# Optimization experiments

Measured on AMD Instinct MI355X. Metric: run time of the kernel, lower is better.

## Reference

```python
import jax, jax.numpy as jnp
import numpy as np

N_FEAT = 1024
N_LAYER = 4  # n_layer + 1 in the original module


def setup_inputs() -> dict:
    key = jax.random.key(0)
    kx, kw, kb = jax.random.split(key, 3)
    x = jax.random.normal(kx, (16384, N_FEAT), dtype=jnp.float32)
    weight_w = jax.random.normal(kw, (N_LAYER, N_FEAT), dtype=jnp.float32)
    weight_b = jax.random.normal(kb, (N_LAYER, N_FEAT), dtype=jnp.float32)
    return {"x": x, "weight_w": weight_w, "weight_b": weight_b}


def reference(x, weight_w, weight_b):
    # Original per layer: x_{i+1} = x0 @ x_i^T @ w_i + b_i + x_i  (per sample).
    # (x0 x_i^T) w = x0 * <x_i, w>, so we use the O(n) equivalent form and
    # never materialize the [B, n, n] outer product.
    x0 = x  # [B, n]
    xi = x0
    for i in range(N_LAYER):
        xiw = jnp.einsum("bn,n->b", xi, weight_w[i])  # [B]
        xi = x0 * xiw[:, None] + weight_b[i][None, :] + xi
    return xi
```

## Files before the change

### kernel.cpp

```cpp
#include <hip/hip_runtime.h>

#define N_FEAT 1024
#define N_LAYER 4
#define R 8

__global__ __launch_bounds__(256) void crossnet_kernel(
    const float* __restrict__ x,
    const float* __restrict__ weight_w,
    const float* __restrict__ weight_b,
    float* __restrict__ out,
    int n_rows) {
  const int wave = threadIdx.x >> 6;
  const int lane = threadIdx.x & 63;
  const int row0 = (blockIdx.x * 4 + wave) * R;
  if (row0 >= n_rows) return;

  const float4* xq = (const float4*)x;
  float4* oq = (float4*)out;

  float4 x0[R * 4];
#pragma unroll
  for (int r = 0; r < R; ++r)
#pragma unroll
    for (int c = 0; c < 4; ++c)
      x0[r * 4 + c] = xq[(size_t)(row0 + r) * 256 + c * 64 + lane];

  float p[R * N_LAYER];
#pragma unroll
  for (int k = 0; k < R * N_LAYER; ++k) p[k] = 0.f;
  float e[N_LAYER] = {0.f, 0.f, 0.f, 0.f};
  float4 csum[4];

#pragma unroll
  for (int c = 0; c < 4; ++c) {
    float4 w[N_LAYER];
#pragma unroll
    for (int i = 0; i < N_LAYER; ++i)
      w[i] = ((const float4*)(weight_w + i * N_FEAT))[c * 64 + lane];

    float4 cum = make_float4(0.f, 0.f, 0.f, 0.f);
#pragma unroll
    for (int i = 0; i < N_LAYER; ++i) {
      if (i > 0)
        e[i] += cum.x * w[i].x + cum.y * w[i].y + cum.z * w[i].z + cum.w * w[i].w;
      float4 b = ((const float4*)(weight_b + i * N_FEAT))[c * 64 + lane];
      cum.x += b.x; cum.y += b.y; cum.z += b.z; cum.w += b.w;
    }
    csum[c] = cum;

#pragma unroll
    for (int r = 0; r < R; ++r) {
      const float4 xv = x0[r * 4 + c];
#pragma unroll
      for (int i = 0; i < N_LAYER; ++i) {
        p[r * N_LAYER + i] += xv.x * w[i].x + xv.y * w[i].y +
                              xv.z * w[i].z + xv.w * w[i].w;
      }
    }
  }

#pragma unroll
  for (int off = 32; off > 0; off >>= 1) {
#pragma unroll
    for (int k = 0; k < R * N_LAYER; ++k) p[k] += __shfl_xor(p[k], off, 64);
#pragma unroll
    for (int i = 1; i < N_LAYER; ++i) e[i] += __shfl_xor(e[i], off, 64);
  }

#pragma unroll
  for (int r = 0; r < R; ++r) {
    float A = 1.f;
#pragma unroll
    for (int i = 0; i < N_LAYER; ++i)
      A += A * p[r * N_LAYER + i] + e[i];

#pragma unroll
    for (int c = 0; c < 4; ++c) {
      const float4 xv = x0[r * 4 + c];
      float4 o;
      o.x = fmaf(xv.x, A, csum[c].x);
      o.y = fmaf(xv.y, A, csum[c].y);
      o.z = fmaf(xv.z, A, csum[c].z);
      o.w = fmaf(xv.w, A, csum[c].w);
      oq[(size_t)(row0 + r) * 256 + c * 64 + lane] = o;
    }
  }
}

extern "C" void kernel_launch(void* const* d_in, const int* in_sizes, int n_in,
                              void* d_out, int out_size, void* d_ws, size_t ws_size,
                              hipStream_t stream) {
  const float* x = (const float*)d_in[0];
  const float* ww = (const float*)d_in[1];
  const float* wb = (const float*)d_in[2];
  float* out = (float*)d_out;

  int n_rows = in_sizes[0] / N_FEAT;
  int rows_per_block = 4 * R;
  int n_blocks = (n_rows + rows_per_block - 1) / rows_per_block;
  crossnet_kernel<<<n_blocks, 256, 0, stream>>>(x, ww, wb, out, n_rows);
}
```

Measured before the change: 119.1 us.

## Split crossnet into reduction kernel and streaming elementwise output kernel

Replaces the single fused kernel, which kept each wave's rows in registers and wrote output directly, with two kernels. The first computes per-row scale factors and the bias cumsum into workspace. The second is a grid-stride elementwise pass that re-reads x and writes the output. This frees registers and gives a simple streaming second pass, at the cost of reading x from memory twice and paying an extra launch.

New measurement: 132.5 us. +11.3%, slower.

```diff
diff --git a/kernel.cpp b/kernel.cpp
--- a/kernel.cpp
+++ b/kernel.cpp
@@ -2,34 +2,39 @@
 
 #define N_FEAT 1024
 #define N_LAYER 4
-#define R 8
+#define R1 8
 
-__global__ __launch_bounds__(256) void crossnet_kernel(
+
+__global__ __launch_bounds__(256) void crossnet_phase1(
     const float* __restrict__ x,
     const float* __restrict__ weight_w,
     const float* __restrict__ weight_b,
-    float* __restrict__ out,
+    float* __restrict__ A_out,
+    float* __restrict__ csum_out,
     int n_rows) {
   const int wave = threadIdx.x >> 6;
   const int lane = threadIdx.x & 63;
-  const int row0 = (blockIdx.x * 4 + wave) * R;
+  const int row0 = (blockIdx.x * 4 + wave) * R1;
+
+  if (blockIdx.x == 0) {
+    const int t = threadIdx.x;
+    float4 c = make_float4(0.f, 0.f, 0.f, 0.f);
+#pragma unroll
+    for (int i = 0; i < N_LAYER; ++i) {
+      const float4 b = ((const float4*)(weight_b + i * N_FEAT))[t];
+      c.x += b.x; c.y += b.y; c.z += b.z; c.w += b.w;
+    }
+    ((float4*)csum_out)[t] = c;
+  }
+
   if (row0 >= n_rows) return;
 
   const float4* xq = (const float4*)x;
-  float4* oq = (float4*)out;
 
-  float4 x0[R * 4];
+  float p[R1 * N_LAYER];
 #pragma unroll
-  for (int r = 0; r < R; ++r)
-#pragma unroll
-    for (int c = 0; c < 4; ++c)
-      x0[r * 4 + c] = xq[(size_t)(row0 + r) * 256 + c * 64 + lane];
-
-  float p[R * N_LAYER];
-#pragma unroll
-  for (int k = 0; k < R * N_LAYER; ++k) p[k] = 0.f;
+  for (int k = 0; k < R1 * N_LAYER; ++k) p[k] = 0.f;
   float e[N_LAYER] = {0.f, 0.f, 0.f, 0.f};
-  float4 csum[4];
 
 #pragma unroll
   for (int c = 0; c < 4; ++c) {
@@ -43,14 +48,13 @@
     for (int i = 0; i < N_LAYER; ++i) {
       if (i > 0)
         e[i] += cum.x * w[i].x + cum.y * w[i].y + cum.z * w[i].z + cum.w * w[i].w;
-      float4 b = ((const float4*)(weight_b + i * N_FEAT))[c * 64 + lane];
+      const float4 b = ((const float4*)(weight_b + i * N_FEAT))[c * 64 + lane];
       cum.x += b.x; cum.y += b.y; cum.z += b.z; cum.w += b.w;
     }
-    csum[c] = cum;
 
 #pragma unroll
-    for (int r = 0; r < R; ++r) {
-      const float4 xv = x0[r * 4 + c];
+    for (int r = 0; r < R1; ++r) {
+      const float4 xv = xq[(size_t)(row0 + r) * 256 + c * 64 + lane];
 #pragma unroll
       for (int i = 0; i < N_LAYER; ++i) {
         p[r * N_LAYER + i] += xv.x * w[i].x + xv.y * w[i].y +
@@ -62,28 +66,44 @@
 #pragma unroll
   for (int off = 32; off > 0; off >>= 1) {
 #pragma unroll
-    for (int k = 0; k < R * N_LAYER; ++k) p[k] += __shfl_xor(p[k], off, 64);
+    for (int k = 0; k < R1 * N_LAYER; ++k) p[k] += __shfl_xor(p[k], off, 64);
 #pragma unroll
     for (int i = 1; i < N_LAYER; ++i) e[i] += __shfl_xor(e[i], off, 64);
   }
 
+  if (lane == 0) {
 #pragma unroll
-  for (int r = 0; r < R; ++r) {
-    float A = 1.f;
+    for (int r = 0; r < R1; ++r) {
+      float A = 1.f;
 #pragma unroll
-    for (int i = 0; i < N_LAYER; ++i)
-      A += A * p[r * N_LAYER + i] + e[i];
+      for (int i = 0; i < N_LAYER; ++i)
+        A += A * p[r * N_LAYER + i] + e[i];
+      A_out[row0 + r] = A;
+    }
+  }
+}
 
-#pragma unroll
-    for (int c = 0; c < 4; ++c) {
-      const float4 xv = x0[r * 4 + c];
-      float4 o;
-      o.x = fmaf(xv.x, A, csum[c].x);
-      o.y = fmaf(xv.y, A, csum[c].y);
-      o.z = fmaf(xv.z, A, csum[c].z);
-      o.w = fmaf(xv.w, A, csum[c].w);
-      oq[(size_t)(row0 + r) * 256 + c * 64 + lane] = o;
-    }
+__global__ __launch_bounds__(256) void crossnet_phase2(
+    const float* __restrict__ x,
+    const float* __restrict__ A_in,
+    const float* __restrict__ csum_in,
+    float* __restrict__ out,
+    int n_q) {
+  const float4* xq = (const float4*)x;
+  const float4* cq = (const float4*)csum_in;
+  float4* oq = (float4*)out;
+
+  const int stride = gridDim.x * 256;
+  for (int q = blockIdx.x * 256 + threadIdx.x; q < n_q; q += stride) {
+    const float a = A_in[q >> 8];
+    const float4 xv = xq[q];
+    const float4 c = cq[q & 255];
+    float4 o;
+    o.x = fmaf(xv.x, a, c.x);
+    o.y = fmaf(xv.y, a, c.y);
+    o.z = fmaf(xv.z, a, c.z);
+    o.w = fmaf(xv.w, a, c.w);
+    oq[q] = o;
   }
 }
 
@@ -95,8 +115,14 @@
   const float* wb = (const float*)d_in[2];
   float* out = (float*)d_out;
 
-  int n_rows = in_sizes[0] / N_FEAT;
-  int rows_per_block = 4 * R;
-  int n_blocks = (n_rows + rows_per_block - 1) / rows_per_block;
-  crossnet_kernel<<<n_blocks, 256, 0, stream>>>(x, ww, wb, out, n_rows);
+  const int n_rows = in_sizes[0] / N_FEAT;
+  float* A_ws = (float*)d_ws;
+  float* csum_ws = A_ws + n_rows;
+
+  const int rows_per_block = 4 * R1;
+  const int n_blocks1 = (n_rows + rows_per_block - 1) / rows_per_block;
+  crossnet_phase1<<<n_blocks1, 256, 0, stream>>>(x, ww, wb, A_ws, csum_ws, n_rows);
+
+  const int n_q = n_rows * 256;
+  crossnet_phase2<<<4096, 256, 0, stream>>>(x, A_ws, csum_ws, out, n_q);
 }
```

## Double-buffer row tiles through LDS with async global-to-LDS loads

Applied to the files above, without the earlier changes.

The kernel no longer keeps 8 rows of x per wave in registers. Each block now walks 4 groups of 8 rows and prefetches the next group into a double-buffered shared-memory tile using global_load_lds, while the current group is reduced and written out. The layer weights and bias-correction terms are loaded once per block and kept in registers. The aim is to cut register pressure and overlap memory reads with compute, at the cost of 64KB of LDS per block, a barrier per group, and relying on the async loads being complete when the barrier is reached.

Measured after the change: 116.6 us. 1.02x faster.

```diff
diff --git a/kernel.cpp b/kernel.cpp
--- a/kernel.cpp
+++ b/kernel.cpp
@@ -2,7 +2,10 @@
 
 #define N_FEAT 1024
 #define N_LAYER 4
-#define R 8
+#define RPG 8
+#define GPB 4
+#define AS1 __attribute__((address_space(1)))
+#define AS3 __attribute__((address_space(3)))
 
 __global__ __launch_bounds__(256) void crossnet_kernel(
     const float* __restrict__ x,
@@ -12,78 +15,101 @@
     int n_rows) {
   const int wave = threadIdx.x >> 6;
   const int lane = threadIdx.x & 63;
-  const int row0 = (blockIdx.x * 4 + wave) * R;
-  if (row0 >= n_rows) return;
 
-  const float4* xq = (const float4*)x;
-  float4* oq = (float4*)out;
+  __shared__ float buf[2][RPG * N_FEAT];
 
-  float4 x0[R * 4];
-#pragma unroll
-  for (int r = 0; r < R; ++r)
-#pragma unroll
-    for (int c = 0; c < 4; ++c)
-      x0[r * 4 + c] = xq[(size_t)(row0 + r) * 256 + c * 64 + lane];
-
-  float p[R * N_LAYER];
-#pragma unroll
-  for (int k = 0; k < R * N_LAYER; ++k) p[k] = 0.f;
+  float4 w[4][N_LAYER];
+  float4 csum[4];
   float e[N_LAYER] = {0.f, 0.f, 0.f, 0.f};
-  float4 csum[4];
-
 #pragma unroll
   for (int c = 0; c < 4; ++c) {
-    float4 w[N_LAYER];
 #pragma unroll
     for (int i = 0; i < N_LAYER; ++i)
-      w[i] = ((const float4*)(weight_w + i * N_FEAT))[c * 64 + lane];
-
+      w[c][i] = ((const float4*)(weight_w + i * N_FEAT))[c * 64 + lane];
     float4 cum = make_float4(0.f, 0.f, 0.f, 0.f);
 #pragma unroll
     for (int i = 0; i < N_LAYER; ++i) {
       if (i > 0)
-        e[i] += cum.x * w[i].x + cum.y * w[i].y + cum.z * w[i].z + cum.w * w[i].w;
-      float4 b = ((const float4*)(weight_b + i * N_FEAT))[c * 64 + lane];
+        e[i] += cum.x * w[c][i].x + cum.y * w[c][i].y +
+                cum.z * w[c][i].z + cum.w * w[c][i].w;
+      const float4 b = ((const float4*)(weight_b + i * N_FEAT))[c * 64 + lane];
       cum.x += b.x; cum.y += b.y; cum.z += b.z; cum.w += b.w;
     }
     csum[c] = cum;
+  }
+#pragma unroll
+  for (int off = 32; off > 0; off >>= 1)
+#pragma unroll
+    for (int i = 1; i < N_LAYER; ++i) e[i] += __shfl_xor(e[i], off, 64);
+
+  const int g0 = blockIdx.x * GPB;
+  if (g0 * RPG >= n_rows) return;
+
+  auto stage = [&](int bsel, int grow) {
+#pragma unroll
+    for (int j = 0; j < 8; ++j) {
+      const float* gsrc = x + (size_t)(grow + 2 * wave + (j >> 2)) * N_FEAT +
+                          ((j & 3) * 64 + lane) * 4;
+      float* ldst = &buf[bsel][(wave * 8 + j) * 256];
+      __builtin_amdgcn_global_load_lds((const AS1 unsigned int*)gsrc,
+                                       (AS3 unsigned int*)ldst, 16, 0, 0);
+    }
+  };
+
+  stage(0, g0 * RPG);
+  __syncthreads();
 
 #pragma unroll
-    for (int r = 0; r < R; ++r) {
-      const float4 xv = x0[r * 4 + c];
+  for (int t = 0; t < GPB; ++t) {
+    const int grow = (g0 + t) * RPG;
+    if (grow >= n_rows) break;
+
+    if (t + 1 < GPB && grow + RPG < n_rows) stage((t + 1) & 1, grow + RPG);
+
+    const float* B = buf[t & 1];
+
+    float4 xv[2][4];
+    float p[2 * N_LAYER];
 #pragma unroll
-      for (int i = 0; i < N_LAYER; ++i) {
-        p[r * N_LAYER + i] += xv.x * w[i].x + xv.y * w[i].y +
-                              xv.z * w[i].z + xv.w * w[i].w;
+    for (int k = 0; k < 2 * N_LAYER; ++k) p[k] = 0.f;
+#pragma unroll
+    for (int r = 0; r < 2; ++r) {
+#pragma unroll
+      for (int c = 0; c < 4; ++c) {
+        xv[r][c] = *(const float4*)&B[(wave * 2 + r) * N_FEAT +
+                                      (c * 64 + lane) * 4];
+#pragma unroll
+        for (int i = 0; i < N_LAYER; ++i) {
+          p[r * N_LAYER + i] += xv[r][c].x * w[c][i].x + xv[r][c].y * w[c][i].y +
+                                xv[r][c].z * w[c][i].z + xv[r][c].w * w[c][i].w;
+        }
       }
     }
-  }
 
 #pragma unroll
-  for (int off = 32; off > 0; off >>= 1) {
+    for (int off = 32; off > 0; off >>= 1)
 #pragma unroll
-    for (int k = 0; k < R * N_LAYER; ++k) p[k] += __shfl_xor(p[k], off, 64);
-#pragma unroll
-    for (int i = 1; i < N_LAYER; ++i) e[i] += __shfl_xor(e[i], off, 64);
-  }
+      for (int k = 0; k < 2 * N_LAYER; ++k) p[k] += __shfl_xor(p[k], off, 64);
 
 #pragma unroll
-  for (int r = 0; r < R; ++r) {
-    float A = 1.f;
+    for (int r = 0; r < 2; ++r) {
+      float A = 1.f;
 #pragma unroll
-    for (int i = 0; i < N_LAYER; ++i)
-      A += A * p[r * N_LAYER + i] + e[i];
+      for (int i = 0; i < N_LAYER; ++i)
+        A += A * p[r * N_LAYER + i] + e[i];
+      const size_t row = grow + wave * 2 + r;
+#pragma unroll
+      for (int c = 0; c < 4; ++c) {
+        float4 o;
+        o.x = fmaf(xv[r][c].x, A, csum[c].x);
+        o.y = fmaf(xv[r][c].y, A, csum[c].y);
+        o.z = fmaf(xv[r][c].z, A, csum[c].z);
+        o.w = fmaf(xv[r][c].w, A, csum[c].w);
+        ((float4*)out)[row * 256 + c * 64 + lane] = o;
+      }
+    }
 
-#pragma unroll
-    for (int c = 0; c < 4; ++c) {
-      const float4 xv = x0[r * 4 + c];
-      float4 o;
-      o.x = fmaf(xv.x, A, csum[c].x);
-      o.y = fmaf(xv.y, A, csum[c].y);
-      o.z = fmaf(xv.z, A, csum[c].z);
-      o.w = fmaf(xv.w, A, csum[c].w);
-      oq[(size_t)(row0 + r) * 256 + c * 64 + lane] = o;
-    }
+    __syncthreads();
   }
 }
 
@@ -95,8 +121,8 @@
   const float* wb = (const float*)d_in[2];
   float* out = (float*)d_out;
 
-  int n_rows = in_sizes[0] / N_FEAT;
-  int rows_per_block = 4 * R;
-  int n_blocks = (n_rows + rows_per_block - 1) / rows_per_block;
+  const int n_rows = in_sizes[0] / N_FEAT;
+  const int rows_per_block = RPG * GPB;
+  const int n_blocks = (n_rows + rows_per_block - 1) / rows_per_block;
   crossnet_kernel<<<n_blocks, 256, 0, stream>>>(x, ww, wb, out, n_rows);
 }
```
